# Performance work log

Measured on AMD Instinct MI355X. Metric: run time of the kernel, lower is better.

## Reference

```python
import jax, jax.numpy as jnp
import numpy as np

NEG_SLOPE = 0.2  # PyG GATConv default leaky_relu slope


def gat_conv(x, src, dst, W, a_src, a_dst, b, num_nodes):
    """One PyG-style GATConv layer (concat over heads).
    x: [N, F_in]; src/dst: [E] (message flows src -> dst);
    W: [F_in, H*C]; a_src/a_dst: [H, C]; b: [H*C].
    """
    H, C = a_src.shape
    h = (x @ W).reshape(num_nodes, H, C)              # [N, H, C]
    alpha_src = jnp.sum(h * a_src, axis=-1)           # [N, H]
    alpha_dst = jnp.sum(h * a_dst, axis=-1)           # [N, H]
    e = jax.nn.leaky_relu(alpha_src[src] + alpha_dst[dst], NEG_SLOPE)  # [E, H]
    # segment softmax over incoming edges of each destination node
    m = jax.ops.segment_max(e, dst, num_segments=num_nodes)            # [N, H]
    ex = jnp.exp(e - m[dst])
    s = jax.ops.segment_sum(ex, dst, num_segments=num_nodes)           # [N, H]
    alpha = ex / (s[dst] + 1e-16)                                      # [E, H]
    msg = h[src] * alpha[:, :, None]                                   # [E, H, C]
    out = jax.ops.segment_sum(msg, dst, num_segments=num_nodes)        # [N, H, C]
    return out.reshape(num_nodes, H * C) + b


def setup_inputs() -> dict:
    key = jax.random.key(0)
    ks = jax.random.split(key, 12)
    N, E, F_in, C, H = 50000, 800000, 256, 64, 8
    x = jax.random.normal(ks[0], (N, F_in), dtype=jnp.float32)
    edge_index = jax.random.randint(ks[1], (2, E), 0, N, dtype=jnp.int64)
    glorot = lambda k, shape: jax.random.normal(k, shape, jnp.float32) * np.sqrt(2.0 / (shape[0] + shape[-1]))
    return {
        "x": x,
        "edge_index": edge_index,
        "W1": glorot(ks[2], (F_in, H * C)),
        "att_src1": glorot(ks[3], (H, C)),
        "att_dst1": glorot(ks[4], (H, C)),
        "b1": jnp.zeros((H * C,), jnp.float32),
        "W2": glorot(ks[5], (H * C, 1 * C)),
        "att_src2": glorot(ks[6], (1, C)),
        "att_dst2": glorot(ks[7], (1, C)),
        "b2": jnp.zeros((C,), jnp.float32),
    }


def reference(x, edge_index, W1, att_src1, att_dst1, b1, W2, att_src2, att_dst2, b2):
    N = x.shape[0]
    # add self-loops (PyG GATConv default add_self_loops=True)
    loops = jnp.arange(N, dtype=edge_index.dtype)
    src = jnp.concatenate([edge_index[0], loops])
    dst = jnp.concatenate([edge_index[1], loops])
    h = gat_conv(x, src, dst, W1, att_src1, att_dst1, b1, N)   # [N, 512]
    h = jax.nn.relu(h)                                         # dropout p=0 -> identity
    out = gat_conv(h, src, dst, W2, att_src2, att_dst2, b2, N) # [N, 64]
    return out
```

## Files before the change

kernel.cpp:

```cpp
#include <hip/hip_runtime.h>
#include <hip/hip_bf16.h>
#include <math.h>
#include <type_traits>

#define NEG_SLOPE 0.2f
#define CAP 64

typedef float f32x4 __attribute__((ext_vector_type(4)));
typedef short s16x8 __attribute__((ext_vector_type(8)));
typedef short s16x4 __attribute__((ext_vector_type(4)));

__device__ __forceinline__ float bf2f(ushort s) {
    union { unsigned u; float f; } cv; cv.u = ((unsigned)s) << 16;
    return cv.f;
}
__device__ __forceinline__ ushort f2bf(float f) {
    __hip_bfloat16 b = __float2bfloat16(f);
    union { __hip_bfloat16 b; ushort u; } cv; cv.b = b;
    return cv.u;
}

__device__ __forceinline__ int edge_val(const int* e, long long i, int is64) {
    return is64 ? e[(size_t)(2 * i)] : e[(size_t)i];
}

__global__ void prep_trans(const float* __restrict__ W1, ushort* __restrict__ W1t, int K1, int N1,
                           const float* __restrict__ W2, ushort* __restrict__ W2t, int K2, int N2) {
    int b = blockIdx.x, tid = threadIdx.x;
    int nbW1 = (K1 * N1 + 255) >> 8;
    if (b < nbW1) {
        int idx = b * 256 + tid;
        if (idx < K1 * N1) {
            int k = idx & (K1 - 1), n = idx / K1;
            W1t[(size_t)n * K1 + k] = f2bf(W1[(size_t)k * N1 + n]);
        }
    } else {
        int idx = (b - nbW1) * 256 + tid;
        if (idx < K2 * N2) {
            int k = idx & (K2 - 1), n = idx / K2;
            W2t[(size_t)n * K2 + k] = f2bf(W2[(size_t)k * N2 + n]);
        }
    }
}

template <typename AT, typename CT, int BM, int BN, int WR, int WC, int H>
__device__ __forceinline__ void gemm_core(int bx, int by,
                                          const AT* __restrict__ A,
                                          const ushort* __restrict__ Bt,
                                          CT* __restrict__ C,
                                          const float* __restrict__ att_s,
                                          const float* __restrict__ att_d,
                                          float* __restrict__ as_,
                                          float* __restrict__ ad_,
                                          int M, int N, int K) {
    constexpr int BK = 64;
    constexpr int WAVES = WR * WC;
    constexpr int THREADS = WAVES * 64;
    constexpr int MT = BM / WR / 16;
    constexpr int NT = 4;
    static_assert(BN == WC * 64, "each wave-col owns one 64-col head");
    __shared__ __align__(16) ushort As[BM][BK + 8];
    __shared__ __align__(16) ushort Bs[BN][BK + 8];

    int tid = threadIdx.x;
    int wid = tid >> 6, lane = tid & 63;
    int wr = wid / WC, wc = wid % WC;
    int bm = by * BM, bn = bx * BN;
    int l15 = lane & 15, l4 = lane >> 4;

    f32x4 acc[MT][NT] = {};

    for (int k0 = 0; k0 < K; k0 += BK) {
        if constexpr (std::is_same_v<AT, float>) {
#pragma unroll
            for (int p = 0; p < BM * BK / (4 * THREADS); ++p) {
                int idx = p * THREADS + tid;
                int r = idx >> 4;
                int kc = (idx & 15) << 2;
                float4 v = make_float4(0.f, 0.f, 0.f, 0.f);
                if (bm + r < M) v = *(const float4*)&A[(size_t)(bm + r) * K + k0 + kc];
                s16x4 pk;
                pk[0] = (short)f2bf(v.x); pk[1] = (short)f2bf(v.y);
                pk[2] = (short)f2bf(v.z); pk[3] = (short)f2bf(v.w);
                *(s16x4*)&As[r][kc] = pk;
            }
        } else {
#pragma unroll
            for (int p = 0; p < BM * BK / (8 * THREADS); ++p) {
                int idx = p * THREADS + tid;
                int r = idx >> 3;
                int kc = (idx & 7) << 3;
                s16x8 v = {};
                if (bm + r < M) v = *(const s16x8*)&A[(size_t)(bm + r) * K + k0 + kc];
                *(s16x8*)&As[r][kc] = v;
            }
        }
#pragma unroll
        for (int p = 0; p < BN * BK / (8 * THREADS); ++p) {
            int idx = p * THREADS + tid;
            int n = idx >> 3;
            int kc = (idx & 7) << 3;
            s16x8 v = *(const s16x8*)&Bt[(size_t)(bn + n) * K + k0 + kc];
            *(s16x8*)&Bs[n][kc] = v;
        }
        __syncthreads();
#pragma unroll
        for (int kk = 0; kk < BK; kk += 32) {
            s16x8 af[MT], bf[NT];
            int kb = kk + (l4 << 3);
#pragma unroll
            for (int mt = 0; mt < MT; ++mt)
                af[mt] = *(const s16x8*)&As[wr * (BM / WR) + mt * 16 + l15][kb];
#pragma unroll
            for (int nt = 0; nt < NT; ++nt)
                bf[nt] = *(const s16x8*)&Bs[wc * 64 + nt * 16 + l15][kb];
#pragma unroll
            for (int mt = 0; mt < MT; ++mt)
#pragma unroll
                for (int nt = 0; nt < NT; ++nt)
                    acc[mt][nt] = __builtin_amdgcn_mfma_f32_16x16x32_bf16(af[mt], bf[nt], acc[mt][nt], 0, 0, 0);
        }
        __syncthreads();
    }

    int head = (bn >> 6) + wc;
    float asv[NT], adv[NT];
#pragma unroll
    for (int nt = 0; nt < NT; ++nt) {
        asv[nt] = att_s[head * 64 + nt * 16 + l15];
        adv[nt] = att_d[head * 64 + nt * 16 + l15];
    }
#pragma unroll
    for (int mt = 0; mt < MT; ++mt) {
#pragma unroll
        for (int j = 0; j < 4; ++j) {
            int r = bm + wr * (BM / WR) + mt * 16 + (l4 << 2) + j;
            float ps = 0.f, pd = 0.f;
#pragma unroll
            for (int nt = 0; nt < NT; ++nt) {
                float v = acc[mt][nt][j];
                ps += v * asv[nt];
                pd += v * adv[nt];
            }
#pragma unroll
            for (int off = 1; off < 16; off <<= 1) {
                ps += __shfl_xor(ps, off);
                pd += __shfl_xor(pd, off);
            }
            if (r < M) {
                if (l15 == 0) {
                    as_[(size_t)r * H + head] = ps;
                    ad_[(size_t)r * H + head] = pd;
                }
#pragma unroll
                for (int nt = 0; nt < NT; ++nt) {
                    size_t ci = (size_t)r * N + bn + wc * 64 + nt * 16 + l15;
                    if constexpr (std::is_same_v<CT, float>) C[ci] = acc[mt][nt][j];
                    else C[ci] = f2bf(acc[mt][nt][j]);
                }
            }
        }
    }
}

__global__ __launch_bounds__(256) void gemm1_scatter(
        const int* __restrict__ ebuf, int E, int Nn, int* __restrict__ counts,
        int* __restrict__ csr, int nGemm,
        const float* __restrict__ A, const ushort* __restrict__ Bt,
        ushort* __restrict__ C, const float* __restrict__ att_s,
        const float* __restrict__ att_d, float* __restrict__ as_,
        float* __restrict__ ad_, int M, int N, int K) {
    int g = blockIdx.x;
    if (g < nGemm) {
        int by = (g & 7) + ((g >> 5) << 3);
        int bx = (g >> 3) & 3;
        gemm_core<float, ushort, 128, 128, 2, 2, 8>(bx, by, A, Bt, C,
                                                    att_s, att_d, as_, ad_, M, N, K);
        return;
    }
    __shared__ int s_is64;
    if (threadIdx.x < 64) {
        int v = ebuf[2 * threadIdx.x + 1];
        unsigned long long bl = __ballot(v != 0);
        if (threadIdx.x == 0) s_is64 = (bl == 0ull) ? 1 : 0;
    }
    __syncthreads();
    int is64 = s_is64;
    int i = (g - nGemm) * 256 + threadIdx.x;
    if (i >= E + Nn) return;
    int s, d;
    if (i < E) {
        s = edge_val(ebuf, i, is64);
        d = edge_val(ebuf, (long long)E + i, is64);
    } else {
        s = i - E; d = s;
    }
    int pos = atomicAdd(&counts[d], 1);
    if (pos < CAP) csr[(size_t)d * CAP + pos] = s;
}

template <typename AT, typename CT, int BM, int BN, int WR, int WC, int H>
__global__ __launch_bounds__(WR * WC * 64) void gemm_mfma(
        const AT* __restrict__ A, const ushort* __restrict__ Bt, CT* __restrict__ C,
        const float* __restrict__ att_s, const float* __restrict__ att_d,
        float* __restrict__ as_, float* __restrict__ ad_, int M, int N, int K) {
    gemm_core<AT, CT, BM, BN, WR, WC, H>(blockIdx.x, blockIdx.y, A, Bt, C,
                                         att_s, att_d, as_, ad_, M, N, K);
}

__global__ __launch_bounds__(256) void gat_fused_l1(
        const ushort* __restrict__ h, const float* __restrict__ as_,
        const float* __restrict__ ad_, const int* __restrict__ counts,
        const int* __restrict__ csr, const float* __restrict__ bias,
        ushort* __restrict__ out1, int N) {
    int n = (blockIdx.x * 256 + threadIdx.x) >> 6;
    if (n >= N) return;
    int l = threadIdx.x & 63;
    size_t base = (size_t)n * CAP;
    int deg = counts[n]; deg = deg > CAP ? CAP : deg;

    int hh = l & 7, e0 = l >> 3;
    float adw = ad_[n * 8 + hh];
    float m = -1e30f, s = 0.f;
    for (int k = e0; k < deg; k += 8) {
        int src = csr[base + k];
        float e = as_[src * 8 + hh] + adw;
        e = e > 0.f ? e : NEG_SLOPE * e;
        float mn = fmaxf(m, e);
        s = s * __expf(m - mn) + __expf(e - mn);
        m = mn;
    }
#pragma unroll
    for (int off = 8; off < 64; off <<= 1) {
        float mo = __shfl_xor(m, off), so = __shfl_xor(s, off);
        float mn = fmaxf(m, mo);
        s = s * __expf(m - mn) + so * __expf(mo - mn);
        m = mn;
    }
    float inv = 1.f / (s + 1e-16f);
    int hd = l >> 3;
    float mh   = __shfl(m, hd);
    float invh = __shfl(inv, hd);
    float adh  = __shfl(adw, hd);

    float acc[8] = {};
    int k = 0;
    for (; k + 4 <= deg; k += 4) {
        int s0 = csr[base + k],     s1 = csr[base + k + 1];
        int s2 = csr[base + k + 2], s3 = csr[base + k + 3];
        s16x8 v0 = *(const s16x8*)&h[((size_t)s0 << 9) + (l << 3)];
        s16x8 v1 = *(const s16x8*)&h[((size_t)s1 << 9) + (l << 3)];
        s16x8 v2 = *(const s16x8*)&h[((size_t)s2 << 9) + (l << 3)];
        s16x8 v3 = *(const s16x8*)&h[((size_t)s3 << 9) + (l << 3)];
        float e0v = as_[s0 * 8 + hd] + adh;
        float e1v = as_[s1 * 8 + hd] + adh;
        float e2v = as_[s2 * 8 + hd] + adh;
        float e3v = as_[s3 * 8 + hd] + adh;
        e0v = e0v > 0.f ? e0v : NEG_SLOPE * e0v;
        e1v = e1v > 0.f ? e1v : NEG_SLOPE * e1v;
        e2v = e2v > 0.f ? e2v : NEG_SLOPE * e2v;
        e3v = e3v > 0.f ? e3v : NEG_SLOPE * e3v;
        float a0 = __expf(e0v - mh);
        float a1 = __expf(e1v - mh);
        float a2 = __expf(e2v - mh);
        float a3 = __expf(e3v - mh);
#pragma unroll
        for (int j = 0; j < 8; ++j)
            acc[j] += a0 * bf2f((ushort)v0[j]) + a1 * bf2f((ushort)v1[j])
                    + a2 * bf2f((ushort)v2[j]) + a3 * bf2f((ushort)v3[j]);
    }
    for (; k < deg; ++k) {
        int s0 = csr[base + k];
        s16x8 v0 = *(const s16x8*)&h[((size_t)s0 << 9) + (l << 3)];
        float e0v = as_[s0 * 8 + hd] + adh;
        e0v = e0v > 0.f ? e0v : NEG_SLOPE * e0v;
        float a0 = __expf(e0v - mh);
#pragma unroll
        for (int j = 0; j < 8; ++j) acc[j] += a0 * bf2f((ushort)v0[j]);
    }
    float4 b0 = *(const float4*)&bias[l * 8];
    float4 b1 = *(const float4*)&bias[l * 8 + 4];
    s16x8 w;
    w[0] = f2bf(fmaxf(acc[0] * invh + b0.x, 0.f));
    w[1] = f2bf(fmaxf(acc[1] * invh + b0.y, 0.f));
    w[2] = f2bf(fmaxf(acc[2] * invh + b0.z, 0.f));
    w[3] = f2bf(fmaxf(acc[3] * invh + b0.w, 0.f));
    w[4] = f2bf(fmaxf(acc[4] * invh + b1.x, 0.f));
    w[5] = f2bf(fmaxf(acc[5] * invh + b1.y, 0.f));
    w[6] = f2bf(fmaxf(acc[6] * invh + b1.z, 0.f));
    w[7] = f2bf(fmaxf(acc[7] * invh + b1.w, 0.f));
    *(s16x8*)&out1[((size_t)n << 9) + (l << 3)] = w;
}

__global__ __launch_bounds__(256) void gat_fused_l2(
        const ushort* __restrict__ h, const float* __restrict__ as_,
        const float* __restrict__ ad_, const int* __restrict__ counts,
        const int* __restrict__ csr, const float* __restrict__ bias,
        float* __restrict__ out, int N) {
    int n = (blockIdx.x * 256 + threadIdx.x) >> 6;
    if (n >= N) return;
    int l = threadIdx.x & 63;
    size_t base = (size_t)n * CAP;
    int deg = counts[n]; deg = deg > CAP ? CAP : deg;
    float adv = ad_[n];

    float m = -1e30f, s = 0.f;
    for (int k = l; k < deg; k += 64) {
        float e = as_[csr[base + k]] + adv;
        e = e > 0.f ? e : NEG_SLOPE * e;
        float mn = fmaxf(m, e);
        s = s * __expf(m - mn) + __expf(e - mn);
        m = mn;
    }
#pragma unroll
    for (int off = 1; off < 64; off <<= 1) {
        float mo = __shfl_xor(m, off), so = __shfl_xor(s, off);
        float mn = fmaxf(m, mo);
        s = s * __expf(m - mn) + so * __expf(mo - mn);
        m = mn;
    }
    float inv = 1.f / (s + 1e-16f);

    int q = l >> 4, c4 = l & 15;
    float a0 = 0.f, a1 = 0.f, a2 = 0.f, a3 = 0.f;
    int k = q;
    for (; k + 12 < deg; k += 16) {
        int sA = csr[base + k],     sB = csr[base + k + 4];
        int sC = csr[base + k + 8], sD = csr[base + k + 12];
        s16x4 vA = *(const s16x4*)&h[((size_t)sA << 6) + (c4 << 2)];
        s16x4 vB = *(const s16x4*)&h[((size_t)sB << 6) + (c4 << 2)];
        s16x4 vC = *(const s16x4*)&h[((size_t)sC << 6) + (c4 << 2)];
        s16x4 vD = *(const s16x4*)&h[((size_t)sD << 6) + (c4 << 2)];
        float eA = as_[sA] + adv, eB = as_[sB] + adv;
        float eC = as_[sC] + adv, eD = as_[sD] + adv;
        eA = eA > 0.f ? eA : NEG_SLOPE * eA;
        eB = eB > 0.f ? eB : NEG_SLOPE * eB;
        eC = eC > 0.f ? eC : NEG_SLOPE * eC;
        eD = eD > 0.f ? eD : NEG_SLOPE * eD;
        float aA = __expf(eA - m), aB = __expf(eB - m);
        float aC = __expf(eC - m), aD = __expf(eD - m);
        a0 += aA * bf2f((ushort)vA[0]) + aB * bf2f((ushort)vB[0])
            + aC * bf2f((ushort)vC[0]) + aD * bf2f((ushort)vD[0]);
        a1 += aA * bf2f((ushort)vA[1]) + aB * bf2f((ushort)vB[1])
            + aC * bf2f((ushort)vC[1]) + aD * bf2f((ushort)vD[1]);
        a2 += aA * bf2f((ushort)vA[2]) + aB * bf2f((ushort)vB[2])
            + aC * bf2f((ushort)vC[2]) + aD * bf2f((ushort)vD[2]);
        a3 += aA * bf2f((ushort)vA[3]) + aB * bf2f((ushort)vB[3])
            + aC * bf2f((ushort)vC[3]) + aD * bf2f((ushort)vD[3]);
    }
    for (; k < deg; k += 4) {
        int sA = csr[base + k];
        s16x4 vA = *(const s16x4*)&h[((size_t)sA << 6) + (c4 << 2)];
        float eA = as_[sA] + adv;
        eA = eA > 0.f ? eA : NEG_SLOPE * eA;
        float aA = __expf(eA - m);
        a0 += aA * bf2f((ushort)vA[0]);
        a1 += aA * bf2f((ushort)vA[1]);
        a2 += aA * bf2f((ushort)vA[2]);
        a3 += aA * bf2f((ushort)vA[3]);
    }
    a0 += __shfl_xor(a0, 16); a0 += __shfl_xor(a0, 32);
    a1 += __shfl_xor(a1, 16); a1 += __shfl_xor(a1, 32);
    a2 += __shfl_xor(a2, 16); a2 += __shfl_xor(a2, 32);
    a3 += __shfl_xor(a3, 16); a3 += __shfl_xor(a3, 32);
    if (q == 0) {
        float4 bv = *(const float4*)&bias[c4 << 2];
        float4 r;
        r.x = a0 * inv + bv.x; r.y = a1 * inv + bv.y;
        r.z = a2 * inv + bv.z; r.w = a3 * inv + bv.w;
        *(float4*)&out[((size_t)n << 6) + (c4 << 2)] = r;
    }
}

extern "C" void kernel_launch(void* const* d_in, const int* in_sizes, int n_in,
                              void* d_out, int out_size, void* d_ws, size_t ws_size,
                              hipStream_t stream) {
    const float* x    = (const float*)d_in[0];
    const int*   ebuf = (const int*)d_in[1];
    const float* W1   = (const float*)d_in[2];
    const float* aS1  = (const float*)d_in[3];
    const float* aD1  = (const float*)d_in[4];
    const float* b1   = (const float*)d_in[5];
    const float* W2   = (const float*)d_in[6];
    const float* aS2  = (const float*)d_in[7];
    const float* aD2  = (const float*)d_in[8];
    const float* b2   = (const float*)d_in[9];
    float* out = (float*)d_out;

    const int F_in = 256, H1 = 8, HC1 = 512, C2 = 64;
    int N = in_sizes[0] / F_in;
    int E = in_sizes[1] / 2;

    char* ws = (char*)d_ws;
    size_t off = 0;
    auto alloc = [&](size_t bytes) -> void* {
        void* p = ws + off;
        off = (off + bytes + 255) & ~(size_t)255;
        return p;
    };
    ushort* h1b    = (ushort*)alloc((size_t)N * HC1 * 2);
    ushort* out1b  = (ushort*)alloc((size_t)N * HC1 * 2);
    float* as1     = (float*)alloc((size_t)N * H1 * 4);
    float* ad1     = (float*)alloc((size_t)N * H1 * 4);
    float* as2     = (float*)alloc((size_t)N * 4);
    float* ad2     = (float*)alloc((size_t)N * 4);
    int*   counts  = (int*)alloc((size_t)N * 4);
    int*   csr     = (int*)alloc((size_t)N * CAP * 4);
    ushort* W1t    = (ushort*)alloc((size_t)F_in * HC1 * 2);
    ushort* W2t    = (ushort*)alloc((size_t)HC1 * C2 * 2);
    ushort* h2b    = h1b;

    int nbW1 = (F_in * HC1 + 255) >> 8;
    int nbW2 = (HC1 * C2 + 255) >> 8;

    hipMemsetAsync(counts, 0, (size_t)N * 4, stream);

    prep_trans<<<nbW1 + nbW2, 256, 0, stream>>>(W1, W1t, F_in, HC1, W2, W2t, HC1, C2);

    {
        int nby = (N + 127) / 128;
        int nbyPad = (nby + 7) & ~7;
        int nGemm = 4 * nbyPad;
        int nScatter = (E + N + 255) / 256;
        gemm1_scatter<<<nGemm + nScatter, 256, 0, stream>>>(
            ebuf, E, N, counts, csr, nGemm,
            x, W1t, h1b, aS1, aD1, as1, ad1, N, HC1, F_in);
    }

    gat_fused_l1<<<(N + 3) / 4, 256, 0, stream>>>(h1b, as1, ad1, counts, csr, b1, out1b, N);

    {
        dim3 g(1, (N + 63) / 64);
        gemm_mfma<ushort, ushort, 64, 64, 4, 1, 1><<<g, 256, 0, stream>>>(
            out1b, W2t, h2b, aS2, aD2, as2, ad2, N, C2, HC1);
    }
    gat_fused_l2<<<(N + 3) / 4, 256, 0, stream>>>(h2b, as2, ad2, counts, csr, b2, out, N);
}
```

Measured before the change: 302.7 us.

## Pre-convert x to bf16 in prep kernel and move edge scatter there

Adds a pass in the prep kernel that converts x from fp32 to bf16 into a reused workspace buffer, and moves the edge scatter/CSR build from the GEMM1 launch into the same prep kernel. GEMM1 now loads bf16 A tiles directly instead of converting fp32 per tile, and it no longer shares its grid with the scatter blocks. The extra full pass over x (read 51MB, write 25MB) has to be paid back by the cheaper GEMM loads. Running the scatter before the GEMM also removes the overlap the two previously had.

```diff
diff --git a/kernel.cpp b/kernel.cpp
--- a/kernel.cpp
+++ b/kernel.cpp
@@ -24,28 +24,71 @@
     return is64 ? e[(size_t)(2 * i)] : e[(size_t)i];
 }
 
-__global__ void prep_trans(const float* __restrict__ W1, ushort* __restrict__ W1t, int K1, int N1,
-                           const float* __restrict__ W2, ushort* __restrict__ W2t, int K2, int N2) {
+__global__ __launch_bounds__(256) void prep_mega(
+        const float* __restrict__ x, ushort* __restrict__ xb, int NX,
+        const float* __restrict__ W1, ushort* __restrict__ W1t, int K1, int N1,
+        const float* __restrict__ W2, ushort* __restrict__ W2t, int K2, int N2,
+        const int* __restrict__ ebuf, int E, int Nn,
+        int* __restrict__ counts, int* __restrict__ csr,
+        int nbX, int nbW1, int nbW2) {
     int b = blockIdx.x, tid = threadIdx.x;
-    int nbW1 = (K1 * N1 + 255) >> 8;
+    if (b < nbX) {
+        int base = (b * 256 + tid) * 8;
+        if (base + 8 <= NX) {
+            float4 v0 = *(const float4*)&x[base];
+            float4 v1 = *(const float4*)&x[base + 4];
+            s16x8 w;
+            w[0] = (short)f2bf(v0.x); w[1] = (short)f2bf(v0.y);
+            w[2] = (short)f2bf(v0.z); w[3] = (short)f2bf(v0.w);
+            w[4] = (short)f2bf(v1.x); w[5] = (short)f2bf(v1.y);
+            w[6] = (short)f2bf(v1.z); w[7] = (short)f2bf(v1.w);
+            *(s16x8*)&xb[base] = w;
+        }
+        return;
+    }
+    b -= nbX;
     if (b < nbW1) {
         int idx = b * 256 + tid;
         if (idx < K1 * N1) {
             int k = idx & (K1 - 1), n = idx / K1;
             W1t[(size_t)n * K1 + k] = f2bf(W1[(size_t)k * N1 + n]);
         }
-    } else {
-        int idx = (b - nbW1) * 256 + tid;
+        return;
+    }
+    b -= nbW1;
+    if (b < nbW2) {
+        int idx = b * 256 + tid;
         if (idx < K2 * N2) {
             int k = idx & (K2 - 1), n = idx / K2;
             W2t[(size_t)n * K2 + k] = f2bf(W2[(size_t)k * N2 + n]);
         }
-    }
-}
-
-template <typename AT, typename CT, int BM, int BN, int WR, int WC, int H>
+        return;
+    }
+    b -= nbW2;
+    __shared__ int s_is64;
+    if (tid < 64) {
+        int v = ebuf[2 * tid + 1];
+        unsigned long long bl = __ballot(v != 0);
+        if (tid == 0) s_is64 = (bl == 0ull) ? 1 : 0;
+    }
+    __syncthreads();
+    int is64 = s_is64;
+    int i = b * 256 + tid;
+    if (i >= E + Nn) return;
+    int s, d;
+    if (i < E) {
+        s = edge_val(ebuf, i, is64);
+        d = edge_val(ebuf, (long long)E + i, is64);
+    } else {
+        s = i - E; d = s;
+    }
+    int pos = atomicAdd(&counts[d], 1);
+    if (pos < CAP) csr[(size_t)d * CAP + pos] = s;
+}
+
+template <typename CT, int BM, int BN, int WR, int WC, int H>
 __device__ __forceinline__ void gemm_core(int bx, int by,
-                                          const AT* __restrict__ A,
+                                          const ushort* __restrict__ A,
                                           const ushort* __restrict__ Bt,
                                           CT* __restrict__ C,
                                           const float* __restrict__ att_s,
@@ -71,29 +114,14 @@
     f32x4 acc[MT][NT] = {};
 
     for (int k0 = 0; k0 < K; k0 += BK) {
-        if constexpr (std::is_same_v<AT, float>) {
-#pragma unroll
-            for (int p = 0; p < BM * BK / (4 * THREADS); ++p) {
-                int idx = p * THREADS + tid;
-                int r = idx >> 4;
-                int kc = (idx & 15) << 2;
-                float4 v = make_float4(0.f, 0.f, 0.f, 0.f);
-                if (bm + r < M) v = *(const float4*)&A[(size_t)(bm + r) * K + k0 + kc];
-                s16x4 pk;
-                pk[0] = (short)f2bf(v.x); pk[1] = (short)f2bf(v.y);
-                pk[2] = (short)f2bf(v.z); pk[3] = (short)f2bf(v.w);
-                *(s16x4*)&As[r][kc] = pk;
-            }
-        } else {
-#pragma unroll
-            for (int p = 0; p < BM * BK / (8 * THREADS); ++p) {
-                int idx = p * THREADS + tid;
-                int r = idx >> 3;
-                int kc = (idx & 7) << 3;
-                s16x8 v = {};
-                if (bm + r < M) v = *(const s16x8*)&A[(size_t)(bm + r) * K + k0 + kc];
-                *(s16x8*)&As[r][kc] = v;
-            }
+#pragma unroll
+        for (int p = 0; p < BM * BK / (8 * THREADS); ++p) {
+            int idx = p * THREADS + tid;
+            int r = idx >> 3;
+            int kc = (idx & 7) << 3;
+            s16x8 v = {};
+            if (bm + r < M) v = *(const s16x8*)&A[(size_t)(bm + r) * K + k0 + kc];
+            *(s16x8*)&As[r][kc] = v;
         }
 #pragma unroll
         for (int p = 0; p < BN * BK / (8 * THREADS); ++p) {
@@ -163,49 +191,24 @@
     }
 }
 
-__global__ __launch_bounds__(256) void gemm1_scatter(
-        const int* __restrict__ ebuf, int E, int Nn, int* __restrict__ counts,
-        int* __restrict__ csr, int nGemm,
-        const float* __restrict__ A, const ushort* __restrict__ Bt,
+__global__ __launch_bounds__(256) void gemm1_mfma(
+        const ushort* __restrict__ A, const ushort* __restrict__ Bt,
         ushort* __restrict__ C, const float* __restrict__ att_s,
         const float* __restrict__ att_d, float* __restrict__ as_,
         float* __restrict__ ad_, int M, int N, int K) {
     int g = blockIdx.x;
-    if (g < nGemm) {
-        int by = (g & 7) + ((g >> 5) << 3);
-        int bx = (g >> 3) & 3;
-        gemm_core<float, ushort, 128, 128, 2, 2, 8>(bx, by, A, Bt, C,
-                                                    att_s, att_d, as_, ad_, M, N, K);
-        return;
-    }
-    __shared__ int s_is64;
-    if (threadIdx.x < 64) {
-        int v = ebuf[2 * threadIdx.x + 1];
-        unsigned long long bl = __ballot(v != 0);
-        if (threadIdx.x == 0) s_is64 = (bl == 0ull) ? 1 : 0;
-    }
-    __syncthreads();
-    int is64 = s_is64;
-    int i = (g - nGemm) * 256 + threadIdx.x;
-    if (i >= E + Nn) return;
-    int s, d;
-    if (i < E) {
-        s = edge_val(ebuf, i, is64);
-        d = edge_val(ebuf, (long long)E + i, is64);
-    } else {
-        s = i - E; d = s;
-    }
-    int pos = atomicAdd(&counts[d], 1);
-    if (pos < CAP) csr[(size_t)d * CAP + pos] = s;
-}
-
-template <typename AT, typename CT, int BM, int BN, int WR, int WC, int H>
+    int by = (g & 7) + ((g >> 5) << 3);
+    int bx = (g >> 3) & 3;
+    gemm_core<ushort, 128, 128, 2, 2, 8>(bx, by, A, Bt, C, att_s, att_d, as_, ad_, M, N, K);
+}
+
+template <typename CT, int BM, int BN, int WR, int WC, int H>
 __global__ __launch_bounds__(WR * WC * 64) void gemm_mfma(
-        const AT* __restrict__ A, const ushort* __restrict__ Bt, CT* __restrict__ C,
+        const ushort* __restrict__ A, const ushort* __restrict__ Bt, CT* __restrict__ C,
         const float* __restrict__ att_s, const float* __restrict__ att_d,
         float* __restrict__ as_, float* __restrict__ ad_, int M, int N, int K) {
-    gemm_core<AT, CT, BM, BN, WR, WC, H>(blockIdx.x, blockIdx.y, A, Bt, C,
-                                         att_s, att_d, as_, ad_, M, N, K);
+    gemm_core<CT, BM, BN, WR, WC, H>(blockIdx.x, blockIdx.y, A, Bt, C,
+                                     att_s, att_d, as_, ad_, M, N, K);
 }
 
 __global__ __launch_bounds__(256) void gat_fused_l1(
@@ -390,6 +393,7 @@
     const int F_in = 256, H1 = 8, HC1 = 512, C2 = 64;
     int N = in_sizes[0] / F_in;
     int E = in_sizes[1] / 2;
+    int NX = N * F_in;
 
     char* ws = (char*)d_ws;
     size_t off = 0;
@@ -409,29 +413,31 @@
     ushort* W1t    = (ushort*)alloc((size_t)F_in * HC1 * 2);
     ushort* W2t    = (ushort*)alloc((size_t)HC1 * C2 * 2);
     ushort* h2b    = h1b;
-
+    ushort* xb     = out1b;
+
+    int nbX  = (NX + 2047) / 2048;
     int nbW1 = (F_in * HC1 + 255) >> 8;
     int nbW2 = (HC1 * C2 + 255) >> 8;
+    int nbScat = (E + N + 255) / 256;
 
     hipMemsetAsync(counts, 0, (size_t)N * 4, stream);
 
-    prep_trans<<<nbW1 + nbW2, 256, 0, stream>>>(W1, W1t, F_in, HC1, W2, W2t, HC1, C2);
+    prep_mega<<<nbX + nbW1 + nbW2 + nbScat, 256, 0, stream>>>(
+        x, xb, NX, W1, W1t, F_in, HC1, W2, W2t, HC1, C2,
+        ebuf, E, N, counts, csr, nbX, nbW1, nbW2);
 
     {
         int nby = (N + 127) / 128;
         int nbyPad = (nby + 7) & ~7;
-        int nGemm = 4 * nbyPad;
-        int nScatter = (E + N + 255) / 256;
-        gemm1_scatter<<<nGemm + nScatter, 256, 0, stream>>>(
-            ebuf, E, N, counts, csr, nGemm,
-            x, W1t, h1b, aS1, aD1, as1, ad1, N, HC1, F_in);
+        gemm1_mfma<<<4 * nbyPad, 256, 0, stream>>>(
+            xb, W1t, h1b, aS1, aD1, as1, ad1, N, HC1, F_in);
     }
 
     gat_fused_l1<<<(N + 3) / 4, 256, 0, stream>>>(h1b, as1, ad1, counts, csr, b1, out1b, N);
 
     {
         dim3 g(1, (N + 63) / 64);
-        gemm_mfma<ushort, ushort, 64, 64, 4, 1, 1><<<g, 256, 0, stream>>>(
+        gemm_mfma<ushort, 64, 64, 4, 1, 1><<<g, 256, 0, stream>>>(
             out1b, W2t, h2b, aS2, aD2, as2, ad2, N, C2, HC1);
     }
     gat_fused_l2<<<(N + 3) / 4, 256, 0, stream>>>(h2b, as2, ad2, counts, csr, b2, out, N);
```

Result: slower. 309.8 us (+2.4%).
